# Kernel tuning notes

Measured on AMD Instinct MI355X. Metric: run time of the kernel, lower is better.

The kernel has to match this reference:

```python
import jax, jax.numpy as jnp
import numpy as np

H = 300  # hidden_size

def _u(key, shape):
    return jax.random.uniform(key, shape, minval=-0.1, maxval=0.1, dtype=jnp.float32)

def setup_inputs() -> dict:
    key = jax.random.key(0)
    ks = jax.random.split(key, 20)
    B, T = 128, 64
    return {
        "local_inputs": jax.random.normal(ks[0], (B, T, 20, 12), dtype=jnp.float32),
        "labels": jax.random.normal(ks[1], (B, T, 1, 1), dtype=jnp.float32),
        "extras": jax.random.normal(ks[2], (B, T, 17, 1), dtype=jnp.float32),
        "DisM": jax.random.uniform(ks[3], (12,), dtype=jnp.float32),
        "AngleM": jax.random.uniform(ks[4], (12,), dtype=jnp.float32),
        # 12 neighbor LSTMCells (input 8 -> hidden 300); W_hh omitted since h0=0
        "W_ih": _u(ks[5], (12, 4 * H, 8)),
        "b_ih": _u(ks[6], (12, 4 * H)),
        "b_hh": _u(ks[7], (12, 4 * H)),
        # target LSTMCell (input 5 -> hidden 300)
        "Wt_ih": _u(ks[8], (4 * H, 5)),
        "bt_ih": _u(ks[9], (4 * H,)),
        "bt_hh": _u(ks[10], (4 * H,)),
        "Att1": _u(ks[11], (600, 200)),
        "ba1": _u(ks[12], (200,)),
        "Att2": _u(ks[13], (202, 1)),
        "ba2": _u(ks[14], (1,)),
        "fuse2": _u(ks[15], (600, 200)),
        "biasf2": _u(ks[16], (200,)),
        "Wout": _u(ks[17], (200, 1)),
        "biasout": _u(ks[18], (1,)),
    }

def _lstm_zero_state(gates):
    # PyTorch LSTMCell gate order i,f,g,o; zero initial (h, c):
    # c' = sigmoid(i)*tanh(g), h' = sigmoid(o)*tanh(c')
    i, f, g, o = jnp.split(gates, 4, axis=-1)
    c = jax.nn.sigmoid(i) * jnp.tanh(g)
    return jax.nn.sigmoid(o) * jnp.tanh(c)

def reference(local_inputs, labels, extras, DisM, AngleM,
              W_ih, b_ih, b_hh, Wt_ih, bt_ih, bt_hh,
              Att1, ba1, Att2, ba2, fuse2, biasf2, Wout, biasout):
    B, T = local_inputs.shape[0], local_inputs.shape[1]
    # Every LSTMCell is called with zero state each timestep -> no recurrence;
    # vectorize over all timesteps and the 12 neighbor channels at once.
    S = local_inputs[:, :, 0:8, :]                                 # [B,T,8,12]
    gates = jnp.einsum('btfc,cgf->btcg', S, W_ih) + b_ih + b_hh    # [B,T,12,1200]
    h = _lstm_zero_state(gates)                                    # [B,T,12,300]
    tgt = extras[:, :, 0:5, 0]                                     # [B,T,5]
    gt = jnp.einsum('btf,gf->btg', tgt, Wt_ih) + bt_ih + bt_hh     # [B,T,1200]
    htarget = _lstm_zero_state(gt)                                 # [B,T,300]
    # attention: per channel, relu(cat[htarget,h_i] @ Att1 + ba1), append wij rows 7,6
    ht12 = jnp.broadcast_to(htarget[:, :, None, :], (B, T, 12, H))
    cat = jnp.concatenate([ht12, h], axis=-1)                      # [B,T,12,600]
    a = jax.nn.relu(jnp.einsum('btcd,de->btce', cat, Att1) + ba1)  # [B,T,12,200]
    wij = jnp.stack([local_inputs[:, :, 7, :], local_inputs[:, :, 6, :]], axis=-1)  # [B,T,12,2]
    fc = jnp.concatenate([a, wij], axis=-1)                        # [B,T,12,202]
    score = jax.nn.relu(jnp.einsum('btcd,do->btco', fc, Att2) + ba2)[..., 0]  # [B,T,12]
    # faithful to source: scores detached (.tolist), softmax over the 12 channels
    # with layout [12,B], then RAW row-major reshape to [B,12] (not a transpose)
    st = jnp.transpose(score, (1, 2, 0))                           # [T,12,B]
    w = jax.nn.softmax(jax.lax.stop_gradient(st), axis=1)          # [T,12,B]
    w = w.reshape(T, B, 12)                                        # raw reshape as in torch
    w = jnp.transpose(w, (1, 0, 2))                                # [B,T,12]
    con = jnp.transpose(h, (0, 1, 3, 2))                           # [B,T,300,12]
    fusion = jnp.sum(con * w[:, :, None, :], axis=-1)              # [B,T,300]
    fusion = jnp.concatenate([fusion, htarget], axis=-1)           # [B,T,600]
    fuse = jnp.einsum('btd,de->bte', fusion, fuse2) + biasf2       # [B,T,200]
    predict = jnp.einsum('btd,do->bto', fuse, Wout) + biasout      # [B,T,1]
    predicts = jnp.transpose(predict, (1, 0, 2))                   # [T,B,1] (list over timesteps)
    labels_out = jnp.transpose(labels[:, :, 0, :], (1, 0, 2))      # [T,B,1]
    return predicts, labels_out
```

## Files before the change

kernel.cpp:

```cpp
#include <hip/hip_runtime.h>
#include <hip/hip_bf16.h>

#define HH   300
#define NB   128
#define NTT  64
#define NP   8192
#define NCH  12
#define KPAD 320
#define NTI2 14

typedef __attribute__((ext_vector_type(8))) short short8;
typedef __attribute__((ext_vector_type(4))) float f32x4;

__device__ __forceinline__ float fsig(float x){
  return __builtin_amdgcn_rcpf(1.f + __expf(-x));
}
__device__ __forceinline__ float ftanh(float x){
  float e = __expf(2.f*x);
  return 1.f - 2.f*__builtin_amdgcn_rcpf(e + 1.f);
}
__device__ __forceinline__ float bf2f(unsigned short u){
  return __uint_as_float(((unsigned)u) << 16);
}
__device__ __forceinline__ unsigned short f2bf(float f){
  __hip_bfloat16 h = __float2bfloat16(f);
  return *reinterpret_cast<unsigned short*>(&h);
}
__device__ __forceinline__ unsigned short rbf(float f){
  return (unsigned short)((__float_as_uint(f) + 0x8000u) >> 16);
}
__device__ __forceinline__ int swzi(int row, int col, int strideShorts){
  int byte = row*(strideShorts*2) + (col<<1);
  byte ^= (row & 7) << 4;
  return byte >> 1;
}

__global__ __launch_bounds__(256) void k_prep(
    const float* __restrict__ Att1, const float* __restrict__ ba1,
    const float* __restrict__ Wih, const float* __restrict__ bih,
    const float* __restrict__ bhh, const float* __restrict__ fuse2,
    const float* __restrict__ bf2, const float* __restrict__ Wout,
    const float* __restrict__ bout, const float* __restrict__ li,
    unsigned short* __restrict__ a1hi2, unsigned short* __restrict__ a1lo2,
    unsigned short* __restrict__ wg3, float* __restrict__ bsum3,
    unsigned short* __restrict__ Sbf, float* __restrict__ kconst)
{
  int bid = blockIdx.x, tid = threadIdx.x;
  if (bid == 1989){
    __shared__ float red[256];
    red[tid] = (tid < 200) ? bf2[tid]*Wout[tid] : 0.f;
    __syncthreads();
    for (int s=128; s>0; s>>=1){
      if (tid < s) red[tid] += red[tid+s];
      __syncthreads();
    }
    if (tid == 0) kconst[0] = red[0] + bout[0];
    return;
  }
  if (bid >= 965){
    int pb0 = (bid - 965) * 8;
    __shared__ float s_li[8*240];
    for (int i = tid; i < 8*240; i += 256)
      s_li[i] = li[(size_t)pb0*240 + i];
    __syncthreads();
    for (int i = tid; i < 8*96; i += 256){
      int pp = i / 96, rem = i - pp*96;
      int c = rem >> 3, f = rem & 7;
      Sbf[((size_t)c*NP + pb0 + pp)*8 + f] = f2bf(s_li[pp*240 + f*12 + c]);
    }
    return;
  }
  int id = bid*256 + tid;
  if (id < 71680){
    int e = id/320, k = id - e*320;
    float v = 0.f;
    if (e < 200 && k < 300){
      v = Att1[(size_t)(300+k)*200 + e];
    } else if (e == 208 && k < 300){
      const float* fr = fuse2 + (size_t)k*200;
      float a = 0.f;
      #pragma unroll 4
      for (int e2=0; e2<200; e2++) a += fr[e2]*Wout[e2];
      v = a;
    }
    a1hi2[id] = f2bf(v);
  } else if (id < 143360){
    int j = id - 71680;
    int e = j/320, k = j - e*320;
    float v = 0.f;
    if (e < 200){
      if (k < 300)       v = Att1[(size_t)k*200 + e];
      else if (k == 300) v = ba1[e];
    } else if (e == 208 && k < 300){
      const float* fr = fuse2 + (size_t)(300+k)*200;
      float a = 0.f;
      #pragma unroll 4
      for (int e2=0; e2<200; e2++) a += fr[e2]*Wout[e2];
      v = a;
    }
    a1lo2[j] = f2bf(v);
  } else if (id < 235520){
    int idx = id - 143360;
    int c = idx / 7680, rem = idx - c*7680;
    int np = rem >> 3, f = rem & 7;
    int G = np / 320, j = np - G*320;
    int off = (G==0) ? 0 : (G==1) ? 600 : 900;
    float v = (j<300) ? Wih[(size_t)c*9600 + (size_t)(off+j)*8 + f] : 0.f;
    wg3[idx] = f2bf(v);
  } else {
    int idx = id - 235520;
    int c = idx / 960, np = idx - c*960;
    int G = np / 320, j = np - G*320;
    int off = (G==0) ? 0 : (G==1) ? 600 : 900;
    bsum3[idx] = (j<300) ? (bih[c*1200+off+j] + bhh[c*1200+off+j]) : 0.f;
  }
}

#define PB 32
__global__ __launch_bounds__(320) void k_ht(
    const float* __restrict__ extras, const float* __restrict__ Wt,
    const float* __restrict__ bti, const float* __restrict__ bth,
    const unsigned short* __restrict__ a1lo2,
    float* __restrict__ ta, float* __restrict__ Tbuf)
{
  int p0 = blockIdx.x * PB;
  int tid = threadIdx.x;
  __shared__ __align__(16) unsigned short s_ht[PB*KPAD];
  __shared__ float s_e[PB][5];
  if (tid < PB*5) s_e[tid/5][tid%5] = extras[(size_t)(p0 + tid/5)*17 + (tid%5)];
  __syncthreads();

  int j = tid;
  if (j < 300){
    float w[15];
    #pragma unroll
    for (int f=0; f<5; f++){
      w[f]    = Wt[(size_t)j*5 + f];
      w[5+f]  = Wt[(size_t)(j+600)*5 + f];
      w[10+f] = Wt[(size_t)(j+900)*5 + f];
    }
    float bi = bti[j]     + bth[j];
    float bg = bti[j+600] + bth[j+600];
    float bo = bti[j+900] + bth[j+900];
    for (int pp=0; pp<PB; pp++){
      float gi=bi, gg=bg, go=bo;
      #pragma unroll
      for (int f=0; f<5; f++){
        float t = s_e[pp][f];
        gi += t*w[f]; gg += t*w[5+f]; go += t*w[10+f];
      }
      float cc = fsig(gi)*ftanh(gg);
      s_ht[swzi(pp, j, KPAD)] = rbf(fsig(go)*ftanh(cc));
    }
  } else {
    unsigned short v = (j == 300) ? (unsigned short)0x3F80 : (unsigned short)0;
    for (int pp=0; pp<PB; pp++)
      s_ht[swzi(pp, j, KPAD)] = v;
  }
  __syncthreads();

  int wave = tid >> 6, lane = tid & 63;
  int lr = lane & 15, lg = lane >> 4;
  f32x4 acc[2][3];
  #pragma unroll
  for (int mt=0; mt<2; mt++)
    #pragma unroll
    for (int t=0; t<3; t++) acc[mt][t] = (f32x4){0.f,0.f,0.f,0.f};
  for (int k0=0; k0<KPAD; k0+=32){
    short8 a[2];
    #pragma unroll
    for (int mt=0; mt<2; mt++)
      a[mt] = *(const short8*)&s_ht[swzi(mt*16 + lr, lg*8 + k0, KPAD)];
    #pragma unroll
    for (int t=0; t<3; t++){
      int nt = wave + t*5;
      if (nt < NTI2){
        short8 b = *(const short8*)(a1lo2 + (size_t)(nt*16 + lr)*KPAD + lg*8 + k0);
        #pragma unroll
        for (int mt=0; mt<2; mt++)
          acc[mt][t] = __builtin_amdgcn_mfma_f32_16x16x32_bf16(a[mt], b, acc[mt][t], 0, 0, 0);
      }
    }
  }
  #pragma unroll
  for (int t=0; t<3; t++){
    int nt = wave + t*5;
    if (nt < 13){
      int e = nt*16 + lr;
      if (e < 200){
        #pragma unroll
        for (int mt=0; mt<2; mt++)
          #pragma unroll
          for (int i=0; i<4; i++)
            ta[(size_t)(p0 + mt*16 + lg*4 + i)*200 + e] = acc[mt][t][i];
      }
    } else if (nt == 13 && lr == 0){
      #pragma unroll
      for (int mt=0; mt<2; mt++)
        #pragma unroll
        for (int i=0; i<4; i++)
          Tbuf[p0 + mt*16 + lg*4 + i] = acc[mt][t][i];
    }
  }
}

__global__ __launch_bounds__(256, 4) void k_hs(
    const float* __restrict__ li, const unsigned short* __restrict__ Sbf,
    const unsigned short* __restrict__ wg3, const float* __restrict__ bsum3,
    const unsigned short* __restrict__ a1hi2, const float* __restrict__ ta,
    const float* __restrict__ att2, const float* __restrict__ ba2,
    float* __restrict__ Hbuf, float* __restrict__ score)
{
  int c  = blockIdx.x >> 7;
  int p0 = (blockIdx.x & 127) << 6;
  int tid = threadIdx.x;
  int wave = tid >> 6, lane = tid & 63;
  int lr = lane & 15, lg = lane >> 4;
  __shared__ __align__(16) unsigned short s_h[64*KPAD];

  short8 z8 = (short8){0,0,0,0,0,0,0,0};
  short8 afrag = z8;
  if (lg == 0)
    afrag = *(const short8*)(Sbf + ((size_t)c*NP + p0 + wave*16 + lr)*8);

  const unsigned short* wgc = wg3 + (size_t)c*960*8;
  const float* bsc = bsum3 + (size_t)c*960;
  f32x4 zero4 = (f32x4){0.f,0.f,0.f,0.f};
  int rowb = wave*16 + lg*4;
  short8 nb0 = z8, nb1 = z8, nb2 = z8;
  if (lg == 0){
    nb0 = *(const short8*)&wgc[(size_t)(      lr)*8];
    nb1 = *(const short8*)&wgc[(size_t)(320 + lr)*8];
    nb2 = *(const short8*)&wgc[(size_t)(640 + lr)*8];
  }
  for (int ch = 0; ch < 20; ch++){
    int n0 = ch*16;
    short8 cb0 = nb0, cb1 = nb1, cb2 = nb2;
    if (ch < 19 && lg == 0){
      int nn = n0 + 16 + lr;
      nb0 = *(const short8*)&wgc[(size_t)(      nn)*8];
      nb1 = *(const short8*)&wgc[(size_t)(320 + nn)*8];
      nb2 = *(const short8*)&wgc[(size_t)(640 + nn)*8];
    }
    f32x4 gi4 = __builtin_amdgcn_mfma_f32_16x16x32_bf16(afrag, cb0, zero4, 0, 0, 0);
    f32x4 gg4 = __builtin_amdgcn_mfma_f32_16x16x32_bf16(afrag, cb1, zero4, 0, 0, 0);
    f32x4 go4 = __builtin_amdgcn_mfma_f32_16x16x32_bf16(afrag, cb2, zero4, 0, 0, 0);
    float bi = bsc[      n0 + lr];
    float bg = bsc[320 + n0 + lr];
    float bo = bsc[640 + n0 + lr];
    #pragma unroll
    for (int i2=0; i2<4; i2++){
      float gi = gi4[i2] + bi;
      float gg = gg4[i2] + bg;
      float go = go4[i2] + bo;
      float cc = fsig(gi)*ftanh(gg);
      float hv = fsig(go)*ftanh(cc);
      s_h[swzi(rowb + i2, n0 + lr, KPAD)] = rbf(hv);
    }
  }
  __syncthreads();

  f32x4 acc[4][4];
  #pragma unroll
  for (int mt=0; mt<4; mt++)
    #pragma unroll
    for (int t4=0; t4<4; t4++) acc[mt][t4] = zero4;
  for (int k0=0; k0<KPAD; k0+=32){
    short8 a[4];
    #pragma unroll
    for (int mt=0; mt<4; mt++)
      a[mt] = *(const short8*)&s_h[swzi(mt*16 + lr, lg*8 + k0, KPAD)];
    #pragma unroll
    for (int t4=0; t4<4; t4++){
      int nt = wave + t4*4;
      if (nt < NTI2){
        short8 b = *(const short8*)(a1hi2 + (size_t)(nt*16 + lr)*KPAD + lg*8 + k0);
        #pragma unroll
        for (int mt=0; mt<4; mt++)
          acc[mt][t4] = __builtin_amdgcn_mfma_f32_16x16x32_bf16(a[mt], b, acc[mt][t4], 0, 0, 0);
      }
    }
  }

  float sacc[4][4];
  #pragma unroll
  for (int mt=0; mt<4; mt++)
    #pragma unroll
    for (int i=0; i<4; i++) sacc[mt][i] = 0.f;
  #pragma unroll
  for (int t4=0; t4<4; t4++){
    int nt = wave + t4*4;
    if (nt < 13){
      int e = nt*16 + lr;
      if (e < 200){
        float a2v = att2[e];
        #pragma unroll
        for (int mt=0; mt<4; mt++){
          #pragma unroll
          for (int i=0; i<4; i++){
            int p = p0 + mt*16 + lg*4 + i;
            float v = acc[mt][t4][i] + ta[(size_t)p*200 + e];
            sacc[mt][i] += fmaxf(v, 0.f) * a2v;
          }
        }
      }
    } else if (nt == 13 && lr == 0){
      #pragma unroll
      for (int mt=0; mt<4; mt++)
        #pragma unroll
        for (int i=0; i<4; i++)
          Hbuf[(size_t)(p0 + mt*16 + lg*4 + i)*NCH + c] = acc[mt][t4][i];
    }
  }
  __syncthreads();
  float* s_red = reinterpret_cast<float*>(s_h);
  #pragma unroll
  for (int mt=0; mt<4; mt++){
    #pragma unroll
    for (int i=0; i<4; i++){
      float s = sacc[mt][i];
      s += __shfl_xor(s, 1);
      s += __shfl_xor(s, 2);
      s += __shfl_xor(s, 4);
      s += __shfl_xor(s, 8);
      if (lr == 0) s_red[wave*64 + mt*16 + lg*4 + i] = s;
    }
  }
  __syncthreads();
  if (tid < 64){
    float r = s_red[tid] + s_red[64+tid] + s_red[128+tid] + s_red[192+tid];
    int p = p0 + tid;
    float w200 = att2[200], w201 = att2[201], b2 = ba2[0];
    float w0 = li[(size_t)p*240 + 84 + c];
    float w1 = li[(size_t)p*240 + 72 + c];
    score[(size_t)p*NCH + c] = fmaxf(r + w0*w200 + w1*w201 + b2, 0.f);
  }
}

__global__ __launch_bounds__(128) void k_sm_final(
    const float* __restrict__ score, const float* __restrict__ Hbuf,
    const float* __restrict__ Tbuf, const float* __restrict__ kconst,
    const float* __restrict__ labels, float* __restrict__ out)
{
  int t = blockIdx.x;
  int b = threadIdx.x;
  __shared__ float ws_f[NCH*NB];
  int p = b*NTT + t;
  const float* s = score + (size_t)p*NCH;
  float v[NCH];
  float m = -1e30f;
  #pragma unroll
  for (int c=0; c<NCH; c++){ v[c] = s[c]; m = fmaxf(m, v[c]); }
  float sum = 0.f;
  #pragma unroll
  for (int c=0; c<NCH; c++){ v[c] = __expf(v[c]-m); sum += v[c]; }
  float inv = __builtin_amdgcn_rcpf(sum);
  #pragma unroll
  for (int c=0; c<NCH; c++)
    ws_f[c*NB + b] = v[c]*inv;
  __syncthreads();
  float acc = Tbuf[p] + kconst[0];
  const float* Hp = Hbuf + (size_t)p*NCH;
  int base = b*NCH;
  #pragma unroll
  for (int c=0; c<NCH; c++)
    acc += ws_f[base + c] * Hp[c];
  out[(size_t)t*NB + b] = acc;
  out[NP + (size_t)t*NB + b] = labels[p];
}

extern "C" void kernel_launch(void* const* d_in, const int* in_sizes, int n_in,
                              void* d_out, int out_size, void* d_ws, size_t ws_size,
                              hipStream_t stream)
{
  const float* li     = (const float*)d_in[0];
  const float* labels = (const float*)d_in[1];
  const float* extras = (const float*)d_in[2];
  const float* Wih    = (const float*)d_in[5];
  const float* bih    = (const float*)d_in[6];
  const float* bhh    = (const float*)d_in[7];
  const float* Wt     = (const float*)d_in[8];
  const float* bti    = (const float*)d_in[9];
  const float* bth    = (const float*)d_in[10];
  const float* Att1   = (const float*)d_in[11];
  const float* ba1    = (const float*)d_in[12];
  const float* Att2   = (const float*)d_in[13];
  const float* ba2    = (const float*)d_in[14];
  const float* fuse2  = (const float*)d_in[15];
  const float* bf2    = (const float*)d_in[16];
  const float* Wout   = (const float*)d_in[17];
  const float* bout   = (const float*)d_in[18];
  float* out = (float*)d_out;

  char* ws = (char*)d_ws;
  float* ta     = (float*)ws;
  float* score  = (float*)(ws + 6553600);
  float* Hbuf   = (float*)(ws + 6946816);
  float* Tbuf   = (float*)(ws + 7340032);
  unsigned short* a1hi2 = (unsigned short*)(ws + 7372800);
  unsigned short* a1lo2 = (unsigned short*)(ws + 7516160);
  unsigned short* wg3   = (unsigned short*)(ws + 7659520);
  float* bsum3  = (float*)(ws + 7843840);
  unsigned short* Sbf   = (unsigned short*)(ws + 7889920);
  float* kconst = (float*)(ws + 9462784);

  k_prep<<<1990, 256, 0, stream>>>(Att1, ba1, Wih, bih, bhh, fuse2, bf2,
                                   Wout, bout, li,
                                   a1hi2, a1lo2, wg3, bsum3, Sbf, kconst);
  k_ht<<<NP/PB, 320, 0, stream>>>(extras, Wt, bti, bth, a1lo2, ta, Tbuf);
  k_hs<<<NCH*128, 256, 0, stream>>>(li, Sbf, wg3, bsum3, a1hi2, ta, Att2, ba2,
                                    Hbuf, score);
  k_sm_final<<<NTT, NB, 0, stream>>>(score, Hbuf, Tbuf, kconst, labels, out);
}
```

Baseline: 190.2 us.

## Double k_hs wave count, fold log2e into gate weights, halve k_ht tile

k_hs now launches 512 threads per block, so eight waves share the LSTM gate phase (two halves of the hidden chunks) and the attention GEMM (two N tiles per wave instead of four). This is meant to raise parallelism and cut per-wave work. The gate weights and biases are pre-scaled by log2(e) or 2*log2(e) so the activations can use exp2 directly. k_ht drops to 16 points per block, giving more blocks with a single M tile. The fuse2·Wout dot in k_prep is vectorized with float4 loads and Wout staged in shared memory. The s_red reduction reads 512 floats, which still fits in the s_h buffer.

```diff
diff --git a/kernel.cpp b/kernel.cpp
--- a/kernel.cpp
+++ b/kernel.cpp
@@ -8,6 +8,8 @@
 #define NCH  12
 #define KPAD 320
 #define NTI2 14
+#define L2E  1.442695041f
+#define L2E2 2.885390082f
 
 typedef __attribute__((ext_vector_type(8))) short short8;
 typedef __attribute__((ext_vector_type(4))) float f32x4;
@@ -18,6 +20,12 @@
 __device__ __forceinline__ float ftanh(float x){
   float e = __expf(2.f*x);
   return 1.f - 2.f*__builtin_amdgcn_rcpf(e + 1.f);
+}
+__device__ __forceinline__ float fsig2(float xs){
+  return __builtin_amdgcn_rcpf(1.f + __builtin_amdgcn_exp2f(-xs));
+}
+__device__ __forceinline__ float ftanh2(float xs){
+  return 1.f - 2.f*__builtin_amdgcn_rcpf(__builtin_amdgcn_exp2f(xs) + 1.f);
 }
 __device__ __forceinline__ float bf2f(unsigned short u){
   return __uint_as_float(((unsigned)u) << 16);
@@ -70,6 +78,9 @@
     }
     return;
   }
+  __shared__ float s_wout[200];
+  for (int i = tid; i < 200; i += 256) s_wout[i] = Wout[i];
+  __syncthreads();
   int id = bid*256 + tid;
   if (id < 71680){
     int e = id/320, k = id - e*320;
@@ -77,11 +88,15 @@
     if (e < 200 && k < 300){
       v = Att1[(size_t)(300+k)*200 + e];
     } else if (e == 208 && k < 300){
-      const float* fr = fuse2 + (size_t)k*200;
-      float a = 0.f;
-      #pragma unroll 4
-      for (int e2=0; e2<200; e2++) a += fr[e2]*Wout[e2];
-      v = a;
+      const float4* fr4 = (const float4*)(fuse2 + (size_t)k*200);
+      float a0=0.f,a1=0.f,a2=0.f,a3=0.f;
+      #pragma unroll 5
+      for (int q=0; q<50; q++){
+        float4 f = fr4[q];
+        float4 w = *(const float4*)&s_wout[q*4];
+        a0 += f.x*w.x; a1 += f.y*w.y; a2 += f.z*w.z; a3 += f.w*w.w;
+      }
+      v = (a0+a1)+(a2+a3);
     }
     a1hi2[id] = f2bf(v);
   } else if (id < 143360){
@@ -92,11 +107,15 @@
       if (k < 300)       v = Att1[(size_t)k*200 + e];
       else if (k == 300) v = ba1[e];
     } else if (e == 208 && k < 300){
-      const float* fr = fuse2 + (size_t)(300+k)*200;
-      float a = 0.f;
-      #pragma unroll 4
-      for (int e2=0; e2<200; e2++) a += fr[e2]*Wout[e2];
-      v = a;
+      const float4* fr4 = (const float4*)(fuse2 + (size_t)(300+k)*200);
+      float a0=0.f,a1=0.f,a2=0.f,a3=0.f;
+      #pragma unroll 5
+      for (int q=0; q<50; q++){
+        float4 f = fr4[q];
+        float4 w = *(const float4*)&s_wout[q*4];
+        a0 += f.x*w.x; a1 += f.y*w.y; a2 += f.z*w.z; a3 += f.w*w.w;
+      }
+      v = (a0+a1)+(a2+a3);
     }
     a1lo2[j] = f2bf(v);
   } else if (id < 235520){
@@ -105,18 +124,20 @@
     int np = rem >> 3, f = rem & 7;
     int G = np / 320, j = np - G*320;
     int off = (G==0) ? 0 : (G==1) ? 600 : 900;
-    float v = (j<300) ? Wih[(size_t)c*9600 + (size_t)(off+j)*8 + f] : 0.f;
+    float sc  = (G==1) ? L2E2 : L2E;
+    float v = (j<300) ? Wih[(size_t)c*9600 + (size_t)(off+j)*8 + f] * sc : 0.f;
     wg3[idx] = f2bf(v);
   } else {
     int idx = id - 235520;
     int c = idx / 960, np = idx - c*960;
     int G = np / 320, j = np - G*320;
     int off = (G==0) ? 0 : (G==1) ? 600 : 900;
-    bsum3[idx] = (j<300) ? (bih[c*1200+off+j] + bhh[c*1200+off+j]) : 0.f;
-  }
-}
-
-#define PB 32
+    float sc  = (G==1) ? L2E2 : L2E;
+    bsum3[idx] = (j<300) ? (bih[c*1200+off+j] + bhh[c*1200+off+j]) * sc : 0.f;
+  }
+}
+
+#define PB 16
 __global__ __launch_bounds__(320) void k_ht(
     const float* __restrict__ extras, const float* __restrict__ Wt,
     const float* __restrict__ bti, const float* __restrict__ bth,
@@ -161,24 +182,17 @@
 
   int wave = tid >> 6, lane = tid & 63;
   int lr = lane & 15, lg = lane >> 4;
-  f32x4 acc[2][3];
-  #pragma unroll
-  for (int mt=0; mt<2; mt++)
-    #pragma unroll
-    for (int t=0; t<3; t++) acc[mt][t] = (f32x4){0.f,0.f,0.f,0.f};
+  f32x4 acc[3];
+  #pragma unroll
+  for (int t=0; t<3; t++) acc[t] = (f32x4){0.f,0.f,0.f,0.f};
   for (int k0=0; k0<KPAD; k0+=32){
-    short8 a[2];
-    #pragma unroll
-    for (int mt=0; mt<2; mt++)
-      a[mt] = *(const short8*)&s_ht[swzi(mt*16 + lr, lg*8 + k0, KPAD)];
+    short8 a = *(const short8*)&s_ht[swzi(lr, lg*8 + k0, KPAD)];
     #pragma unroll
     for (int t=0; t<3; t++){
       int nt = wave + t*5;
       if (nt < NTI2){
         short8 b = *(const short8*)(a1lo2 + (size_t)(nt*16 + lr)*KPAD + lg*8 + k0);
-        #pragma unroll
-        for (int mt=0; mt<2; mt++)
-          acc[mt][t] = __builtin_amdgcn_mfma_f32_16x16x32_bf16(a[mt], b, acc[mt][t], 0, 0, 0);
+        acc[t] = __builtin_amdgcn_mfma_f32_16x16x32_bf16(a, b, acc[t], 0, 0, 0);
       }
     }
   }
@@ -189,22 +203,18 @@
       int e = nt*16 + lr;
       if (e < 200){
         #pragma unroll
-        for (int mt=0; mt<2; mt++)
-          #pragma unroll
-          for (int i=0; i<4; i++)
-            ta[(size_t)(p0 + mt*16 + lg*4 + i)*200 + e] = acc[mt][t][i];
+        for (int i=0; i<4; i++)
+          ta[(size_t)(p0 + lg*4 + i)*200 + e] = acc[t][i];
       }
     } else if (nt == 13 && lr == 0){
       #pragma unroll
-      for (int mt=0; mt<2; mt++)
-        #pragma unroll
-        for (int i=0; i<4; i++)
-          Tbuf[p0 + mt*16 + lg*4 + i] = acc[mt][t][i];
-    }
-  }
-}
-
-__global__ __launch_bounds__(256, 4) void k_hs(
+      for (int i=0; i<4; i++)
+        Tbuf[p0 + lg*4 + i] = acc[t][i];
+    }
+  }
+}
+
+__global__ __launch_bounds__(512, 6) void k_hs(
     const float* __restrict__ li, const unsigned short* __restrict__ Sbf,
     const unsigned short* __restrict__ wg3, const float* __restrict__ bsum3,
     const unsigned short* __restrict__ a1hi2, const float* __restrict__ ta,
@@ -219,24 +229,27 @@
   __shared__ __align__(16) unsigned short s_h[64*KPAD];
 
   short8 z8 = (short8){0,0,0,0,0,0,0,0};
+  int mt1 = wave & 3;
+  int chb = (wave >> 2) * 10;
   short8 afrag = z8;
   if (lg == 0)
-    afrag = *(const short8*)(Sbf + ((size_t)c*NP + p0 + wave*16 + lr)*8);
+    afrag = *(const short8*)(Sbf + ((size_t)c*NP + p0 + mt1*16 + lr)*8);
 
   const unsigned short* wgc = wg3 + (size_t)c*960*8;
   const float* bsc = bsum3 + (size_t)c*960;
   f32x4 zero4 = (f32x4){0.f,0.f,0.f,0.f};
-  int rowb = wave*16 + lg*4;
+  int rowb = mt1*16 + lg*4;
   short8 nb0 = z8, nb1 = z8, nb2 = z8;
   if (lg == 0){
-    nb0 = *(const short8*)&wgc[(size_t)(      lr)*8];
-    nb1 = *(const short8*)&wgc[(size_t)(320 + lr)*8];
-    nb2 = *(const short8*)&wgc[(size_t)(640 + lr)*8];
-  }
-  for (int ch = 0; ch < 20; ch++){
-    int n0 = ch*16;
+    int nr = chb*16 + lr;
+    nb0 = *(const short8*)&wgc[(size_t)(      nr)*8];
+    nb1 = *(const short8*)&wgc[(size_t)(320 + nr)*8];
+    nb2 = *(const short8*)&wgc[(size_t)(640 + nr)*8];
+  }
+  for (int ch = 0; ch < 10; ch++){
+    int n0 = (chb + ch)*16;
     short8 cb0 = nb0, cb1 = nb1, cb2 = nb2;
-    if (ch < 19 && lg == 0){
+    if (ch < 9 && lg == 0){
       int nn = n0 + 16 + lr;
       nb0 = *(const short8*)&wgc[(size_t)(      nn)*8];
       nb1 = *(const short8*)&wgc[(size_t)(320 + nn)*8];
@@ -250,34 +263,34 @@
     float bo = bsc[640 + n0 + lr];
     #pragma unroll
     for (int i2=0; i2<4; i2++){
-      float gi = gi4[i2] + bi;
-      float gg = gg4[i2] + bg;
-      float go = go4[i2] + bo;
-      float cc = fsig(gi)*ftanh(gg);
-      float hv = fsig(go)*ftanh(cc);
-      s_h[swzi(rowb + i2, n0 + lr, KPAD)] = rbf(hv);
-    }
-  }
-  __syncthreads();
-
-  f32x4 acc[4][4];
+      float si = fsig2(gi4[i2] + bi);
+      float tg = ftanh2(gg4[i2] + bg);
+      float cc = si*tg;
+      float tc = ftanh2(cc * L2E2);
+      float so = fsig2(go4[i2] + bo);
+      s_h[swzi(rowb + i2, n0 + lr, KPAD)] = rbf(so*tc);
+    }
+  }
+  __syncthreads();
+
+  f32x4 acc[4][2];
   #pragma unroll
   for (int mt=0; mt<4; mt++)
     #pragma unroll
-    for (int t4=0; t4<4; t4++) acc[mt][t4] = zero4;
+    for (int t=0; t<2; t++) acc[mt][t] = zero4;
   for (int k0=0; k0<KPAD; k0+=32){
     short8 a[4];
     #pragma unroll
     for (int mt=0; mt<4; mt++)
       a[mt] = *(const short8*)&s_h[swzi(mt*16 + lr, lg*8 + k0, KPAD)];
     #pragma unroll
-    for (int t4=0; t4<4; t4++){
-      int nt = wave + t4*4;
+    for (int t=0; t<2; t++){
+      int nt = wave + t*8;
       if (nt < NTI2){
         short8 b = *(const short8*)(a1hi2 + (size_t)(nt*16 + lr)*KPAD + lg*8 + k0);
         #pragma unroll
         for (int mt=0; mt<4; mt++)
-          acc[mt][t4] = __builtin_amdgcn_mfma_f32_16x16x32_bf16(a[mt], b, acc[mt][t4], 0, 0, 0);
+          acc[mt][t] = __builtin_amdgcn_mfma_f32_16x16x32_bf16(a[mt], b, acc[mt][t], 0, 0, 0);
       }
     }
   }
@@ -288,8 +301,8 @@
     #pragma unroll
     for (int i=0; i<4; i++) sacc[mt][i] = 0.f;
   #pragma unroll
-  for (int t4=0; t4<4; t4++){
-    int nt = wave + t4*4;
+  for (int t=0; t<2; t++){
+    int nt = wave + t*8;
     if (nt < 13){
       int e = nt*16 + lr;
       if (e < 200){
@@ -299,7 +312,7 @@
           #pragma unroll
           for (int i=0; i<4; i++){
             int p = p0 + mt*16 + lg*4 + i;
-            float v = acc[mt][t4][i] + ta[(size_t)p*200 + e];
+            float v = acc[mt][t][i] + ta[(size_t)p*200 + e];
             sacc[mt][i] += fmaxf(v, 0.f) * a2v;
           }
         }
@@ -309,7 +322,7 @@
       for (int mt=0; mt<4; mt++)
         #pragma unroll
         for (int i=0; i<4; i++)
-          Hbuf[(size_t)(p0 + mt*16 + lg*4 + i)*NCH + c] = acc[mt][t4][i];
+          Hbuf[(size_t)(p0 + mt*16 + lg*4 + i)*NCH + c] = acc[mt][t][i];
     }
   }
   __syncthreads();
@@ -328,7 +341,9 @@
   }
   __syncthreads();
   if (tid < 64){
-    float r = s_red[tid] + s_red[64+tid] + s_red[128+tid] + s_red[192+tid];
+    float r = 0.f;
+    #pragma unroll
+    for (int w8=0; w8<8; w8++) r += s_red[w8*64 + tid];
     int p = p0 + tid;
     float w200 = att2[200], w201 = att2[201], b2 = ba2[0];
     float w0 = li[(size_t)p*240 + 84 + c];
@@ -408,7 +423,7 @@
                                    Wout, bout, li,
                                    a1hi2, a1lo2, wg3, bsum3, Sbf, kconst);
   k_ht<<<NP/PB, 320, 0, stream>>>(extras, Wt, bti, bth, a1lo2, ta, Tbuf);
-  k_hs<<<NCH*128, 256, 0, stream>>>(li, Sbf, wg3, bsum3, a1hi2, ta, Att2, ba2,
+  k_hs<<<NCH*128, 512, 0, stream>>>(li, Sbf, wg3, bsum3, a1hi2, ta, Att2, ba2,
                                     Hbuf, score);
   k_sm_final<<<NTT, NB, 0, stream>>>(score, Hbuf, Tbuf, kconst, labels, out);
 }
```

New measurement: 172.8 us. 1.1x faster.
